# Kernel optimization log

Hardware: AMD Instinct MI355X
Metric: run time of the kernel (lower is better)

The kernel has to match this reference:

```python
import jax, jax.numpy as jnp
import numpy as np

EPS = 1e-5
NEG_SLOPE = 0.2

def _linear(x, w, b):
    return x @ w.T + b

def _seg_softmax(a, dst, n):
    # numerically stable softmax over edges grouped by destination node
    m = jax.ops.segment_max(a, dst, num_segments=n)
    e = jnp.exp(a - m[dst])
    s = jax.ops.segment_sum(e, dst, num_segments=n)
    return e / (s[dst] + 1e-16)

def _gat(x, src, dst, n, w, a_src, a_dst, b):
    # PyG GATConv, heads=1: h = xW^T; alpha = LeakyReLU(a_s.h_src + a_d.h_dst)
    h = x @ w.T                                   # [N,H]
    al_s = (h * a_src).sum(-1)                    # [N]
    al_d = (h * a_dst).sum(-1)                    # [N]
    alpha = jax.nn.leaky_relu(al_s[src] + al_d[dst], NEG_SLOPE)  # [E]
    attn = _seg_softmax(alpha, dst, n)
    out = jax.ops.segment_sum(attn[:, None] * h[src], dst, num_segments=n)
    return out + b

def _bn(x, g, b):
    # BatchNorm over the node dimension (training-style batch stats, eval dropout)
    mu = x.mean(0)
    var = x.var(0)
    return (x - mu) * jax.lax.rsqrt(var + EPS) * g + b

def setup_inputs() -> dict:
    key = jax.random.key(0)
    N, E, SAT, NEI, H, OUT = 50000, 1600000, 32, 32, 128, 16
    ks = jax.random.split(key, 26)
    p = lambda k, shape, s=0.05: jax.random.normal(k, shape, jnp.float32) * s
    return {
        "x": jax.random.normal(ks[0], (N, SAT + NEI), jnp.float32),
        "edge_index": jax.random.randint(ks[1], (2, E), 0, N, jnp.int32),
        "sat_w": p(ks[2], (H, SAT)), "sat_b": jnp.zeros((H,), jnp.float32),
        "neigh_w": p(ks[3], (H, NEI)), "neigh_b": jnp.zeros((H,), jnp.float32),
        "fus_w": p(ks[4], (1, 2 * H)), "fus_b": jnp.zeros((1,), jnp.float32),
        "w1": p(ks[5], (H, H)), "as1": p(ks[6], (H,)), "ad1": p(ks[7], (H,)), "b1": jnp.zeros((H,), jnp.float32),
        "g1": jnp.ones((H,), jnp.float32), "be1": jnp.zeros((H,), jnp.float32),
        "w2": p(ks[8], (H, H)), "as2": p(ks[9], (H,)), "ad2": p(ks[10], (H,)), "b2": jnp.zeros((H,), jnp.float32),
        "g2": jnp.ones((H,), jnp.float32), "be2": jnp.zeros((H,), jnp.float32),
        "fc1_w": p(ks[11], (H, H)), "fc1_b": jnp.zeros((H,), jnp.float32),
        "fc2_w": p(ks[12], (OUT, H)), "fc2_b": jnp.zeros((OUT,), jnp.float32),
    }

def reference(x, edge_index, sat_w, sat_b, neigh_w, neigh_b, fus_w, fus_b,
              w1, as1, ad1, b1, g1, be1, w2, as2, ad2, b2, g2, be2,
              fc1_w, fc1_b, fc2_w, fc2_b):
    n = x.shape[0]
    sat_dim = sat_w.shape[1]
    sat = jax.nn.relu(_linear(x[:, :sat_dim], sat_w, sat_b))
    nei = jax.nn.relu(_linear(x[:, sat_dim:], neigh_w, neigh_b))
    gate = jax.nn.sigmoid(_linear(jnp.concatenate([sat, nei], axis=1), fus_w, fus_b))
    h = gate * sat + (1.0 - gate) * nei
    # GATConv adds self-loops by default
    loops = jnp.arange(n, dtype=edge_index.dtype)
    src = jnp.concatenate([edge_index[0], loops])
    dst = jnp.concatenate([edge_index[1], loops])
    res = h
    h = jax.nn.relu(_bn(_gat(h, src, dst, n, w1, as1, ad1, b1), g1, be1)) + res
    res = h
    h = jax.nn.relu(_bn(_gat(h, src, dst, n, w2, as2, ad2, b2), g2, be2)) + res
    h = jax.nn.relu(_linear(h, fc1_w, fc1_b))
    return _linear(h, fc2_w, fc2_b)
```

## Files before the change

kernel.cpp:

```cpp
#include <hip/hip_runtime.h>

#define H 128

typedef __attribute__((ext_vector_type(8))) short bf16x8;
typedef __attribute__((ext_vector_type(4))) float f32x4;

__device__ __forceinline__ float bf2f(unsigned short u) {
    return __uint_as_float(((unsigned)u) << 16);
}
__device__ __forceinline__ unsigned short f2bf(float f) {
    unsigned u = __float_as_uint(f);
    unsigned r = (u + 0x7fffu + ((u >> 16) & 1u)) >> 16;
    return (unsigned short)r;
}
__device__ __forceinline__ unsigned pack2bf(float a, float b) {
    return (unsigned)f2bf(a) | ((unsigned)f2bf(b) << 16);
}

__global__ void fuse_kernel(const float* __restrict__ x,
                            const float* __restrict__ sat_w, const float* __restrict__ sat_b,
                            const float* __restrict__ neigh_w, const float* __restrict__ neigh_b,
                            const float* __restrict__ fus_w, const float* __restrict__ fus_b,
                            unsigned short* __restrict__ h0b, int N) {
    __shared__ unsigned smem[8512];
    __shared__ float reds[4][64];
    unsigned* a_lds = smem;
    unsigned* w_lds = smem + 2304;
    int tid = threadIdx.x;
    int base = blockIdx.x * 64;
    for (int i = tid; i < 64 * 32; i += 256) {
        int n = i >> 5, kp = i & 31;
        int gn = base + n;
        float2 v = (gn < N) ? *(const float2*)(x + (size_t)gn * 64 + kp * 2) : make_float2(0.f, 0.f);
        a_lds[n * 36 + kp] = pack2bf(v.x, v.y);
    }
    for (int i = tid; i < 256 * 16; i += 256) {
        int r = i >> 4, kp = i & 15;
        const float* wsrc = (r < 128) ? (sat_w + (size_t)r * 32) : (neigh_w + (size_t)(r - 128) * 32);
        float2 v = *(const float2*)(wsrc + kp * 2);
        w_lds[r * 20 + kp] = pack2bf(v.x, v.y);
    }
    __syncthreads();
    int lane = tid & 63;
    int wv = tid >> 6;
    int lr = lane & 15, lk = lane >> 4;
    f32x4 accS[4][2], accN[4][2];
#pragma unroll
    for (int r = 0; r < 4; ++r)
#pragma unroll
        for (int t = 0; t < 2; ++t) {
            accS[r][t] = (f32x4){0.f, 0.f, 0.f, 0.f};
            accN[r][t] = (f32x4){0.f, 0.f, 0.f, 0.f};
        }
    bf16x8 afS[4], afN[4];
#pragma unroll
    for (int r = 0; r < 4; ++r) {
        afS[r] = *(const bf16x8*)&a_lds[(r * 16 + lr) * 36 + lk * 4];
        afN[r] = *(const bf16x8*)&a_lds[(r * 16 + lr) * 36 + 16 + lk * 4];
    }
#pragma unroll
    for (int t = 0; t < 2; ++t) {
        bf16x8 bS = *(const bf16x8*)&w_lds[(wv * 32 + t * 16 + lr) * 20 + lk * 4];
        bf16x8 bN = *(const bf16x8*)&w_lds[(128 + wv * 32 + t * 16 + lr) * 20 + lk * 4];
#pragma unroll
        for (int r = 0; r < 4; ++r) {
            accS[r][t] = __builtin_amdgcn_mfma_f32_16x16x32_bf16(afS[r], bS, accS[r][t], 0, 0, 0);
            accN[r][t] = __builtin_amdgcn_mfma_f32_16x16x32_bf16(afN[r], bN, accN[r][t], 0, 0, 0);
        }
    }
    __syncthreads();
    unsigned short* cst = (unsigned short*)smem;
#pragma unroll
    for (int t = 0; t < 2; ++t) {
        int col = wv * 32 + t * 16 + lr;
        float sb = sat_b[col], nb = neigh_b[col];
#pragma unroll
        for (int r = 0; r < 4; ++r) {
#pragma unroll
            for (int j = 0; j < 4; ++j) {
                int srow = r * 16 + lk * 4 + j;
                cst[srow * 266 + col] = f2bf(fmaxf(accS[r][t][j] + sb, 0.f));
                cst[srow * 266 + 133 + col] = f2bf(fmaxf(accN[r][t][j] + nb, 0.f));
            }
        }
    }
    __syncthreads();
    int node = tid & 63;
    int part = tid >> 6;
    float ps = 0.f;
#pragma unroll
    for (int k = 0; k < 32; ++k) {
        int col = part * 32 + k;
        ps += bf2f(cst[node * 266 + col]) * fus_w[col]
            + bf2f(cst[node * 266 + 133 + col]) * fus_w[128 + col];
    }
    reds[part][node] = ps;
    __syncthreads();
    float tot = reds[0][node] + reds[1][node] + reds[2][node] + reds[3][node];
    float g = 1.f / (1.f + __expf(-(tot + fus_b[0])));
    if (base + node < N) {
        unsigned* op = (unsigned*)h0b + (size_t)(base + node) * 64 + part * 16;
#pragma unroll
        for (int kp = 0; kp < 16; ++kp) {
            int col = part * 32 + kp * 2;
            float o0 = g * bf2f(cst[node * 266 + col]) + (1.f - g) * bf2f(cst[node * 266 + 133 + col]);
            float o1 = g * bf2f(cst[node * 266 + col + 1]) + (1.f - g) * bf2f(cst[node * 266 + 134 + col]);
            op[kp] = pack2bf(o0, o1);
        }
    }
}

template <int TAG, int MODE>
__global__ void gemm128m(const void* __restrict__ inv, const float* __restrict__ w,
                         const float* __restrict__ bias, int do_relu,
                         unsigned short* __restrict__ outb, int N,
                         const float* __restrict__ a_sp, const float* __restrict__ a_dp,
                         float* __restrict__ al_s, float* __restrict__ al_d,
                         const float* __restrict__ bns, const unsigned short* __restrict__ resb,
                         unsigned* __restrict__ yout) {
    __shared__ unsigned a_lds[64 * 68];
    __shared__ unsigned w_lds[128 * 68];
    __shared__ float reds[4][64];
    __shared__ float redd[4][64];
    int tid = threadIdx.x;
    int base = blockIdx.x * 64;
    for (int i = tid; i < 64 * 64; i += 256) {
        int n = i >> 6, kp = i & 63;
        int gn = base + n;
        unsigned p = 0u;
        if (gn < N) {
            if (MODE == 1) {
                p = ((const unsigned*)inv)[(size_t)gn * 64 + kp];
            } else {
                float2 v = *(const float2*)((const float*)inv + (size_t)gn * 128 + kp * 2);
                float2 sc = ((const float2*)bns)[kp];
                float2 sh = ((const float2*)(bns + 128))[kp];
                ushort2 rr = ((const ushort2*)(resb + (size_t)gn * 128))[kp];
                float y0 = fmaxf(v.x * sc.x + sh.x, 0.f) + bf2f(rr.x);
                float y1 = fmaxf(v.y * sc.y + sh.y, 0.f) + bf2f(rr.y);
                p = pack2bf(y0, y1);
                if (yout) yout[(size_t)gn * 64 + kp] = p;
            }
        }
        a_lds[n * 68 + kp] = p;
    }
    for (int i = tid; i < 128 * 64; i += 256) {
        int c = i >> 6, kp = i & 63;
        float2 v = *(const float2*)(w + (size_t)c * 128 + kp * 2);
        w_lds[c * 68 + kp] = pack2bf(v.x, v.y);
    }
    __syncthreads();
    int lane = tid & 63;
    int wv = tid >> 6;
    int lr = lane & 15;
    int lk = lane >> 4;
    f32x4 acc[4][2];
#pragma unroll
    for (int r = 0; r < 4; ++r)
#pragma unroll
        for (int t = 0; t < 2; ++t) acc[r][t] = (f32x4){0.f, 0.f, 0.f, 0.f};
    for (int c = 0; c < 4; ++c) {
        bf16x8 af[4], bfr[2];
#pragma unroll
        for (int r = 0; r < 4; ++r)
            af[r] = *(const bf16x8*)&a_lds[(r * 16 + lr) * 68 + c * 16 + lk * 4];
#pragma unroll
        for (int t = 0; t < 2; ++t)
            bfr[t] = *(const bf16x8*)&w_lds[(wv * 32 + t * 16 + lr) * 68 + c * 16 + lk * 4];
#pragma unroll
        for (int r = 0; r < 4; ++r)
#pragma unroll
            for (int t = 0; t < 2; ++t)
                acc[r][t] = __builtin_amdgcn_mfma_f32_16x16x32_bf16(af[r], bfr[t], acc[r][t], 0, 0, 0);
    }
    __syncthreads();
    unsigned short* cst = (unsigned short*)a_lds;
#pragma unroll
    for (int t = 0; t < 2; ++t) {
        int col = wv * 32 + t * 16 + lr;
        float bv = bias ? bias[col] : 0.f;
#pragma unroll
        for (int r = 0; r < 4; ++r) {
#pragma unroll
            for (int j = 0; j < 4; ++j) {
                float v = acc[r][t][j] + bv;
                if (do_relu) v = fmaxf(v, 0.f);
                cst[(r * 16 + lk * 4 + j) * 136 + col] = f2bf(v);
            }
        }
    }
    __syncthreads();
    for (int i = tid; i < 64 * 64; i += 256) {
        int n = i >> 6, kp = i & 63;
        int gn = base + n;
        if (gn < N) ((unsigned*)outb)[(size_t)gn * 64 + kp] = a_lds[n * 68 + kp];
    }
    if (a_sp) {
        int node = tid & 63;
        int part = tid >> 6;
        float ps = 0.f, pd = 0.f;
        int kb = part * 32;
        const unsigned short* xr = cst + node * 136 + kb;
#pragma unroll
        for (int k = 0; k < 32; ++k) {
            float v = bf2f(xr[k]);
            ps += v * a_sp[kb + k];
            pd += v * a_dp[kb + k];
        }
        reds[part][node] = ps;
        redd[part][node] = pd;
        __syncthreads();
        if (tid < 64) {
            int gn = base + tid;
            if (gn < N) {
                al_s[gn] = reds[0][tid] + reds[1][tid] + reds[2][tid] + reds[3][tid];
                al_d[gn] = redd[0][tid] + redd[1][tid] + redd[2][tid] + redd[3][tid];
            }
        }
    }
}

#define PBMAX 6400
#define NBSTR 256
__global__ void pack_bucket(const int* __restrict__ src, const int* __restrict__ dst,
                            unsigned* __restrict__ pk2, int* __restrict__ cntBB,
                            int* __restrict__ offBB, int E, int PB) {
    __shared__ unsigned opk[PBMAX];
    __shared__ unsigned opk2[PBMAX];
    __shared__ int lcnt[256];
    __shared__ int tmp[256];
    int tid = threadIdx.x;
    int blk = blockIdx.x;
    int e0 = blk * PB;
    int n = min(PB, E - e0);
    if (n < 0) n = 0;
    lcnt[tid] = 0;
    __syncthreads();
    for (int i = tid; i < n; i += 256) {
        int s = src[e0 + i];
        int d = dst[e0 + i];
        unsigned p = ((unsigned)d << 16) | (unsigned)s;
        opk[i] = p;
        atomicAdd(&lcnt[d >> 8], 1);
    }
    __syncthreads();
    int v = lcnt[tid];
    tmp[tid] = v;
    __syncthreads();
    for (int off = 1; off < 256; off <<= 1) {
        int u = (tid >= off) ? tmp[tid - off] : 0;
        __syncthreads();
        tmp[tid] += u;
        __syncthreads();
    }
    int excl = tmp[tid] - v;
    cntBB[(size_t)blk * NBSTR + tid] = v;
    offBB[(size_t)blk * NBSTR + tid] = excl;
    lcnt[tid] = excl;
    __syncthreads();
    for (int i = tid; i < n; i += 256) {
        unsigned p = opk[i];
        int pos = atomicAdd(&lcnt[(p >> 16) >> 8], 1);
        opk2[pos] = p;
    }
    __syncthreads();
    for (int i = tid; i < n; i += 256) pk2[e0 + i] = opk2[i];
}

__global__ void bucket_base(const int* __restrict__ cntBB, int* __restrict__ bbase,
                            int* __restrict__ rowptr, float* __restrict__ accum,
                            int E, int N, int NBLK) {
    __shared__ int tmp[256];
    int tid = threadIdx.x;
    for (int i = tid; i < 4096; i += 256) accum[i] = 0.f;
    int tot = 0;
    for (int blk = 0; blk < NBLK; ++blk) tot += cntBB[(size_t)blk * NBSTR + tid];
    tmp[tid] = tot;
    __syncthreads();
    for (int off = 1; off < 256; off <<= 1) {
        int u = (tid >= off) ? tmp[tid - off] : 0;
        __syncthreads();
        tmp[tid] += u;
        __syncthreads();
    }
    bbase[tid] = tmp[tid] - tot;
    if (tid == 0) rowptr[N] = E;
}

#define BCAP 10240
__global__ void scatter_sort2(const unsigned* __restrict__ pk2, const int* __restrict__ cntBB,
                              const int* __restrict__ offBB, const int* __restrict__ bbase,
                              int* __restrict__ ssrc, int* __restrict__ rowptr,
                              int N, int PB) {
    __shared__ int segoff[257];
    __shared__ int segsrc[256];
    __shared__ int lcur[256];
    __shared__ int tmp[256];
    __shared__ int osrc[BCAP];
    int b = blockIdx.x;
    int d0 = b << 8;
    int tid = threadIdx.x;
    int c = cntBB[(size_t)tid * NBSTR + b];
    segsrc[tid] = tid * PB + offBB[(size_t)tid * NBSTR + b];
    tmp[tid] = c;
    lcur[tid] = 0;
    __syncthreads();
    for (int off = 1; off < 256; off <<= 1) {
        int u = (tid >= off) ? tmp[tid - off] : 0;
        __syncthreads();
        tmp[tid] += u;
        __syncthreads();
    }
    segoff[tid] = tmp[tid] - c;
    if (tid == 255) segoff[256] = tmp[255];
    __syncthreads();
    int cntb = segoff[256];
    for (int i = tid; i < cntb; i += 256) {
        int lo = 0, hi = 255;
        while (lo < hi) { int mid = (lo + hi + 1) >> 1; if (segoff[mid] <= i) lo = mid; else hi = mid - 1; }
        unsigned p = pk2[segsrc[lo] + (i - segoff[lo])];
        atomicAdd(&lcur[(int)(p >> 16) - d0], 1);
    }
    __syncthreads();
    int v = lcur[tid];
    tmp[tid] = v;
    __syncthreads();
    for (int off = 1; off < 256; off <<= 1) {
        int u = (tid >= off) ? tmp[tid - off] : 0;
        __syncthreads();
        tmp[tid] += u;
        __syncthreads();
    }
    int excl = tmp[tid] - v;
    int gbase = bbase[b];
    if (d0 + tid < N) rowptr[d0 + tid] = gbase + excl;
    lcur[tid] = excl;
    __syncthreads();
    for (int i = tid; i < cntb; i += 256) {
        int lo = 0, hi = 255;
        while (lo < hi) { int mid = (lo + hi + 1) >> 1; if (segoff[mid] <= i) lo = mid; else hi = mid - 1; }
        unsigned p = pk2[segsrc[lo] + (i - segoff[lo])];
        int pos = atomicAdd(&lcur[(int)(p >> 16) - d0], 1);
        osrc[pos] = (int)(p & 0xFFFFu);
    }
    __syncthreads();
    for (int i = tid; i < cntb; i += 256) ssrc[gbase + i] = osrc[i];
}

template <int TAG>
__global__ void gat_agg(const int* __restrict__ rowptr, const int* __restrict__ ssrc,
                        const float* __restrict__ al_s, const float* __restrict__ al_d,
                        const unsigned short* __restrict__ hb, float* __restrict__ out,
                        float* __restrict__ accum8, int N) {
    __shared__ int s_sv[4][64];
    __shared__ float s_ev[4][64];
    __shared__ float ys[4][128];
    __shared__ float yq[4][128];
    int tid = threadIdx.x;
    int wiw = tid >> 6;
    int w = (blockIdx.x * blockDim.x + tid) >> 6;
    int lane = tid & 63;
    int sub = lane >> 5;
    int fl = lane & 31;
    float a0 = 0.f, a1 = 0.f, a2 = 0.f, a3 = 0.f;
    float ss = 0.f;
    if (w < N) {
        int beg = rowptr[w], end = rowptr[w + 1];
        float ald = al_d[w];
        float a_self = al_s[w] + ald;
        a_self = (a_self > 0.f) ? a_self : 0.2f * a_self;
        float m = a_self;
        for (int e = beg + lane; e < end; e += 64) {
            float a = al_s[ssrc[e]] + ald;
            a = (a > 0.f) ? a : 0.2f * a;
            m = fmaxf(m, a);
        }
        for (int off = 32; off; off >>= 1) m = fmaxf(m, __shfl_xor(m, off));
        for (int base = beg; base < end; base += 64) {
            int nch = min(64, end - base);
            int sv = 0;
            float ev = 0.f;
            if (lane < nch) {
                sv = ssrc[base + lane];
                float a = al_s[sv] + ald;
                a = (a > 0.f) ? a : 0.2f * a;
                ev = __expf(a - m);
            }
            ss += ev;
            s_sv[wiw][lane] = sv;
            s_ev[wiw][lane] = ev;
            for (int j0 = 0; j0 < nch; j0 += 8) {
                ushort4 hv[4];
                float evv[4];
#pragma unroll
                for (int jj = 0; jj < 4; ++jj) {
                    int j = j0 + 2 * jj + sub;
                    bool ok = j < nch;
                    int svj = ok ? s_sv[wiw][j] : 0;
                    evv[jj] = ok ? s_ev[wiw][j] : 0.f;
                    hv[jj] = ((const ushort4*)(hb + (size_t)svj * H))[fl];
                }
#pragma unroll
                for (int jj = 0; jj < 4; ++jj) {
                    a0 += evv[jj] * bf2f(hv[jj].x);
                    a1 += evv[jj] * bf2f(hv[jj].y);
                    a2 += evv[jj] * bf2f(hv[jj].z);
                    a3 += evv[jj] * bf2f(hv[jj].w);
                }
            }
        }
        for (int off = 32; off; off >>= 1) ss += __shfl_xor(ss, off);
        a0 += __shfl_xor(a0, 32);
        a1 += __shfl_xor(a1, 32);
        a2 += __shfl_xor(a2, 32);
        a3 += __shfl_xor(a3, 32);
        float ev_self = __expf(a_self - m);
        ss += ev_self;
        ushort4 hs = ((const ushort4*)(hb + (size_t)w * H))[fl];
        a0 += ev_self * bf2f(hs.x);
        a1 += ev_self * bf2f(hs.y);
        a2 += ev_self * bf2f(hs.z);
        a3 += ev_self * bf2f(hs.w);
        float inv = 1.f / (ss + 1e-16f);
        a0 *= inv; a1 *= inv; a2 *= inv; a3 *= inv;
        if (sub == 0) {
            ((float4*)(out + (size_t)w * H))[fl] = make_float4(a0, a1, a2, a3);
        }
    }
    if (sub == 0) {
        float4 yy = (w < N) ? make_float4(a0, a1, a2, a3) : make_float4(0.f, 0.f, 0.f, 0.f);
        ((float4*)&ys[wiw][0])[fl] = yy;
        ((float4*)&yq[wiw][0])[fl] = make_float4(yy.x * yy.x, yy.y * yy.y, yy.z * yy.z, yy.w * yy.w);
    }
    __syncthreads();
    if (tid < 128) {
        float s = ys[0][tid] + ys[1][tid] + ys[2][tid] + ys[3][tid];
        float q = yq[0][tid] + yq[1][tid] + yq[2][tid] + yq[3][tid];
        float* ac = accum8 + (size_t)(blockIdx.x & 7) * 256;
        atomicAdd(ac + tid, s);
        atomicAdd(ac + 128 + tid, q);
    }
}

__global__ void bn_finalize(const float* __restrict__ accum8, const float* __restrict__ g,
                            const float* __restrict__ be, float* __restrict__ bns, int N) {
    int tid = threadIdx.x;
    if (tid >= 128) return;
    float s = 0.f, q = 0.f;
#pragma unroll
    for (int c = 0; c < 8; ++c) {
        s += accum8[c * 256 + tid];
        q += accum8[c * 256 + 128 + tid];
    }
    float Ninv = 1.f / (float)N;
    float mu = s * Ninv;
    float var = q * Ninv - mu * mu;
    float rsig = rsqrtf(var + 1e-5f);
    float sc = rsig * g[tid];
    bns[tid] = sc;
    bns[128 + tid] = be[tid] - mu * sc;
}

__global__ void fc2_kernel(const unsigned short* __restrict__ in, const float* __restrict__ w,
                           const float* __restrict__ b, float* __restrict__ out,
                           int N, int OUT) {
    __shared__ float wsm[16 * 132];
    __shared__ float xs[16][129];
    int tid = threadIdx.x;
    for (int i = tid; i < OUT * H; i += 256) {
        int o = i >> 7, k = i & 127;
        wsm[o * 132 + k] = w[i];
    }
    int nb = blockIdx.x * 16;
    for (int i = tid; i < 16 * 128; i += 256) {
        int n = i >> 7, k = i & 127;
        int gn = nb + n;
        xs[n][k] = (gn < N) ? bf2f(in[(size_t)gn * H + k]) : 0.f;
    }
    __syncthreads();
    int o = tid & 15;
    int nn = tid >> 4;
    int n = nb + nn;
    if (n >= N || o >= OUT) return;
    const float* xr = xs[nn];
    const float* wr = wsm + o * 132;
    float acc = b[o];
#pragma unroll 8
    for (int k = 0; k < H; k += 4) {
        acc += xr[k] * wr[k] + xr[k + 1] * wr[k + 1] + xr[k + 2] * wr[k + 2] + xr[k + 3] * wr[k + 3];
    }
    out[(size_t)n * OUT + o] = acc;
}


extern "C" void kernel_launch(void* const* d_in, const int* in_sizes, int n_in,
                              void* d_out, int out_size, void* d_ws, size_t ws_size,
                              hipStream_t stream) {
    const float* x       = (const float*)d_in[0];
    const int*   ei      = (const int*)d_in[1];
    const float* sat_w   = (const float*)d_in[2];
    const float* sat_b   = (const float*)d_in[3];
    const float* neigh_w = (const float*)d_in[4];
    const float* neigh_b = (const float*)d_in[5];
    const float* fus_w   = (const float*)d_in[6];
    const float* fus_b   = (const float*)d_in[7];
    const float* w1      = (const float*)d_in[8];
    const float* as1     = (const float*)d_in[9];
    const float* ad1     = (const float*)d_in[10];
    const float* g1      = (const float*)d_in[12];
    const float* be1     = (const float*)d_in[13];
    const float* w2      = (const float*)d_in[14];
    const float* as2     = (const float*)d_in[15];
    const float* ad2     = (const float*)d_in[16];
    const float* g2      = (const float*)d_in[18];
    const float* be2     = (const float*)d_in[19];
    const float* fc1_w   = (const float*)d_in[20];
    const float* fc1_b   = (const float*)d_in[21];
    const float* fc2_w   = (const float*)d_in[22];
    const float* fc2_b   = (const float*)d_in[23];

    int N = in_sizes[0] / 64;
    int E = in_sizes[1] / 2;
    int OUT = in_sizes[23];
    int PB = (E + 255) / 256;
    int NBUKET = (N + 255) >> 8;

    float* ws    = (float*)d_ws;
    float* h0    = ws;
    float* hA    = h0 + (size_t)N * H;
    float* agg   = hA + (size_t)N * H;
    float* al_s  = agg + (size_t)N * H;
    float* al_d  = al_s + N;
    float* accum = al_d + N;
    float* bns1  = accum + 4096;
    float* bns2  = bns1 + 256;
    int* rowptr  = (int*)(bns2 + 256);
    int* cntBB   = rowptr + (N + 1);
    int* offBB   = cntBB + 256 * NBSTR;
    int* bbase   = offBB + 256 * NBSTR;
    int* ssrc    = bbase + 256;
    unsigned* pk2= (unsigned*)(ssrc + E);
    unsigned* y1b= pk2 + E;
    unsigned short* hAb = (unsigned short*)hA;
    unsigned short* h0b = (unsigned short*)(hA + (size_t)N * 64);

    const int* srcp = ei;
    const int* dstp = ei + E;

    dim3 b256(256);
    int gGemm = (N + 63) / 64;
    int gWaveN = (N + 3) / 4;

    fuse_kernel<<<gGemm, b256, 0, stream>>>(x, sat_w, sat_b, neigh_w, neigh_b, fus_w, fus_b, h0b, N);

    pack_bucket<<<256, b256, 0, stream>>>(srcp, dstp, pk2, cntBB, offBB, E, PB);
    bucket_base<<<1, b256, 0, stream>>>(cntBB, bbase, rowptr, accum, E, N, 256);
    scatter_sort2<<<NBUKET, b256, 0, stream>>>(pk2, cntBB, offBB, bbase, ssrc, rowptr, N, PB);

    gemm128m<1, 1><<<gGemm, b256, 0, stream>>>(h0b, w1, nullptr, 0, hAb, N, as1, ad1, al_s, al_d,
                                               nullptr, nullptr, nullptr);
    gat_agg<1><<<gWaveN, b256, 0, stream>>>(rowptr, ssrc, al_s, al_d, hAb, agg, accum, N);
    bn_finalize<<<1, 128, 0, stream>>>(accum, g1, be1, bns1, N);

    gemm128m<2, 2><<<gGemm, b256, 0, stream>>>(agg, w2, nullptr, 0, hAb, N, as2, ad2, al_s, al_d,
                                               bns1, h0b, y1b);
    gat_agg<2><<<gWaveN, b256, 0, stream>>>(rowptr, ssrc, al_s, al_d, hAb, h0, accum + 2048, N);
    bn_finalize<<<1, 128, 0, stream>>>(accum + 2048, g2, be2, bns2, N);

    gemm128m<3, 2><<<gGemm, b256, 0, stream>>>(h0, fc1_w, fc1_b, 1, hAb, N, nullptr, nullptr,
                                               nullptr, nullptr, bns2, (const unsigned short*)y1b,
                                               nullptr);
    fc2_kernel<<<(N + 15) / 16, b256, 0, stream>>>(hAb, fc2_w, fc2_b, (float*)d_out, N, OUT);
}
```

Baseline: 352.7 us.

## Fuse BN finalize into GEMM, transpose bucket counts, stage bucket edges in LDS

Removes the two single-block bn_finalize launches by having each MODE-2 GEMM block recompute the BatchNorm scale and shift from the accumulated sums into shared memory. Transposes the cntBB/offBB layout so bucket_base can do a wave-parallel coalesced reduction and scatter_sort2 reads contiguous rows. scatter_sort2 now copies each bucket's edge segments into LDS once instead of running a binary search and a global reload in both passes. This adds another 40KB of LDS per scatter block, which may lower occupancy, and every GEMM block redundantly repeats the small BN computation.

Result: slower. 374.7 us (+6.2%).

```diff
diff --git a/kernel.cpp b/kernel.cpp
--- a/kernel.cpp
+++ b/kernel.cpp
@@ -116,14 +116,33 @@
                          unsigned short* __restrict__ outb, int N,
                          const float* __restrict__ a_sp, const float* __restrict__ a_dp,
                          float* __restrict__ al_s, float* __restrict__ al_d,
-                         const float* __restrict__ bns, const unsigned short* __restrict__ resb,
-                         unsigned* __restrict__ yout) {
+                         const float* __restrict__ accum8, const float* __restrict__ gvec,
+                         const float* __restrict__ bevec,
+                         const unsigned short* __restrict__ resb, unsigned* __restrict__ yout) {
     __shared__ unsigned a_lds[64 * 68];
     __shared__ unsigned w_lds[128 * 68];
     __shared__ float reds[4][64];
     __shared__ float redd[4][64];
+    __shared__ float sc_l[128], sh_l[128];
     int tid = threadIdx.x;
     int base = blockIdx.x * 64;
+    if (MODE == 2) {
+        if (tid < 128) {
+            float s = 0.f, q = 0.f;
+#pragma unroll
+            for (int c = 0; c < 8; ++c) {
+                s += accum8[c * 256 + tid];
+                q += accum8[c * 256 + 128 + tid];
+            }
+            float Ninv = 1.f / (float)N;
+            float mu = s * Ninv;
+            float var = q * Ninv - mu * mu;
+            float sc = rsqrtf(var + 1e-5f) * gvec[tid];
+            sc_l[tid] = sc;
+            sh_l[tid] = bevec[tid] - mu * sc;
+        }
+        __syncthreads();
+    }
     for (int i = tid; i < 64 * 64; i += 256) {
         int n = i >> 6, kp = i & 63;
         int gn = base + n;
@@ -133,8 +152,8 @@
                 p = ((const unsigned*)inv)[(size_t)gn * 64 + kp];
             } else {
                 float2 v = *(const float2*)((const float*)inv + (size_t)gn * 128 + kp * 2);
-                float2 sc = ((const float2*)bns)[kp];
-                float2 sh = ((const float2*)(bns + 128))[kp];
+                float2 sc = ((const float2*)sc_l)[kp];
+                float2 sh = ((const float2*)sh_l)[kp];
                 ushort2 rr = ((const ushort2*)(resb + (size_t)gn * 128))[kp];
                 float y0 = fmaxf(v.x * sc.x + sh.x, 0.f) + bf2f(rr.x);
                 float y1 = fmaxf(v.y * sc.y + sh.y, 0.f) + bf2f(rr.y);
@@ -254,8 +273,8 @@
         __syncthreads();
     }
     int excl = tmp[tid] - v;
-    cntBB[(size_t)blk * NBSTR + tid] = v;
-    offBB[(size_t)blk * NBSTR + tid] = excl;
+    cntBB[(size_t)tid * NBSTR + blk] = v;
+    offBB[(size_t)tid * NBSTR + blk] = excl;
     lcnt[tid] = excl;
     __syncthreads();
     for (int i = tid; i < n; i += 256) {
@@ -269,13 +288,20 @@
 
 __global__ void bucket_base(const int* __restrict__ cntBB, int* __restrict__ bbase,
                             int* __restrict__ rowptr, float* __restrict__ accum,
-                            int E, int N, int NBLK) {
+                            int E, int N) {
+    __shared__ int tot[256];
     __shared__ int tmp[256];
-    int tid = threadIdx.x;
+    int tid = threadIdx.x, wv = tid >> 6, lane = tid & 63;
     for (int i = tid; i < 4096; i += 256) accum[i] = 0.f;
-    int tot = 0;
-    for (int blk = 0; blk < NBLK; ++blk) tot += cntBB[(size_t)blk * NBSTR + tid];
-    tmp[tid] = tot;
+    for (int r = wv; r < 256; r += 4) {
+        int s = 0;
+        for (int i = lane; i < 256; i += 64) s += cntBB[(size_t)r * NBSTR + i];
+        for (int off = 32; off; off >>= 1) s += __shfl_xor(s, off);
+        if (lane == 0) tot[r] = s;
+    }
+    __syncthreads();
+    int v = tot[tid];
+    tmp[tid] = v;
     __syncthreads();
     for (int off = 1; off < 256; off <<= 1) {
         int u = (tid >= off) ? tmp[tid - off] : 0;
@@ -283,7 +309,7 @@
         tmp[tid] += u;
         __syncthreads();
     }
-    bbase[tid] = tmp[tid] - tot;
+    bbase[tid] = tmp[tid] - v;
     if (tid == 0) rowptr[N] = E;
 }
 
@@ -294,14 +320,17 @@
                               int N, int PB) {
     __shared__ int segoff[257];
     __shared__ int segsrc[256];
+    __shared__ int segcnt[256];
     __shared__ int lcur[256];
     __shared__ int tmp[256];
+    __shared__ unsigned opk[BCAP];
     __shared__ int osrc[BCAP];
     int b = blockIdx.x;
     int d0 = b << 8;
     int tid = threadIdx.x;
-    int c = cntBB[(size_t)tid * NBSTR + b];
-    segsrc[tid] = tid * PB + offBB[(size_t)tid * NBSTR + b];
+    int c = cntBB[(size_t)b * NBSTR + tid];
+    segcnt[tid] = c;
+    segsrc[tid] = tid * PB + offBB[(size_t)b * NBSTR + tid];
     tmp[tid] = c;
     lcur[tid] = 0;
     __syncthreads();
@@ -311,16 +340,18 @@
         tmp[tid] += u;
         __syncthreads();
     }
-    segoff[tid] = tmp[tid] - c;
+    segoff[tid] = tmp[tid] - segcnt[tid];
     if (tid == 255) segoff[256] = tmp[255];
     __syncthreads();
     int cntb = segoff[256];
-    for (int i = tid; i < cntb; i += 256) {
-        int lo = 0, hi = 255;
-        while (lo < hi) { int mid = (lo + hi + 1) >> 1; if (segoff[mid] <= i) lo = mid; else hi = mid - 1; }
-        unsigned p = pk2[segsrc[lo] + (i - segoff[lo])];
-        atomicAdd(&lcur[(int)(p >> 16) - d0], 1);
-    }
+    int wv = tid >> 6, lane = tid & 63;
+    for (int s = wv; s < 256; s += 4) {
+        int sc = segcnt[s], so = segoff[s], gs = segsrc[s];
+        for (int i = lane; i < sc; i += 64) opk[so + i] = pk2[gs + i];
+    }
+    __syncthreads();
+    for (int i = tid; i < cntb; i += 256)
+        atomicAdd(&lcur[(opk[i] >> 16) & 255], 1);
     __syncthreads();
     int v = lcur[tid];
     tmp[tid] = v;
@@ -337,10 +368,8 @@
     lcur[tid] = excl;
     __syncthreads();
     for (int i = tid; i < cntb; i += 256) {
-        int lo = 0, hi = 255;
-        while (lo < hi) { int mid = (lo + hi + 1) >> 1; if (segoff[mid] <= i) lo = mid; else hi = mid - 1; }
-        unsigned p = pk2[segsrc[lo] + (i - segoff[lo])];
-        int pos = atomicAdd(&lcur[(int)(p >> 16) - d0], 1);
+        unsigned p = opk[i];
+        int pos = atomicAdd(&lcur[(p >> 16) & 255], 1);
         osrc[pos] = (int)(p & 0xFFFFu);
     }
     __syncthreads();
@@ -442,25 +471,6 @@
     }
 }
 
-__global__ void bn_finalize(const float* __restrict__ accum8, const float* __restrict__ g,
-                            const float* __restrict__ be, float* __restrict__ bns, int N) {
-    int tid = threadIdx.x;
-    if (tid >= 128) return;
-    float s = 0.f, q = 0.f;
-#pragma unroll
-    for (int c = 0; c < 8; ++c) {
-        s += accum8[c * 256 + tid];
-        q += accum8[c * 256 + 128 + tid];
-    }
-    float Ninv = 1.f / (float)N;
-    float mu = s * Ninv;
-    float var = q * Ninv - mu * mu;
-    float rsig = rsqrtf(var + 1e-5f);
-    float sc = rsig * g[tid];
-    bns[tid] = sc;
-    bns[128 + tid] = be[tid] - mu * sc;
-}
-
 __global__ void fc2_kernel(const unsigned short* __restrict__ in, const float* __restrict__ w,
                            const float* __restrict__ b, float* __restrict__ out,
                            int N, int OUT) {
@@ -532,9 +542,7 @@
     float* al_s  = agg + (size_t)N * H;
     float* al_d  = al_s + N;
     float* accum = al_d + N;
-    float* bns1  = accum + 4096;
-    float* bns2  = bns1 + 256;
-    int* rowptr  = (int*)(bns2 + 256);
+    int* rowptr  = (int*)(accum + 4096);
     int* cntBB   = rowptr + (N + 1);
     int* offBB   = cntBB + 256 * NBSTR;
     int* bbase   = offBB + 256 * NBSTR;
@@ -554,21 +562,19 @@
     fuse_kernel<<<gGemm, b256, 0, stream>>>(x, sat_w, sat_b, neigh_w, neigh_b, fus_w, fus_b, h0b, N);
 
     pack_bucket<<<256, b256, 0, stream>>>(srcp, dstp, pk2, cntBB, offBB, E, PB);
-    bucket_base<<<1, b256, 0, stream>>>(cntBB, bbase, rowptr, accum, E, N, 256);
+    bucket_base<<<1, b256, 0, stream>>>(cntBB, bbase, rowptr, accum, E, N);
     scatter_sort2<<<NBUKET, b256, 0, stream>>>(pk2, cntBB, offBB, bbase, ssrc, rowptr, N, PB);
 
     gemm128m<1, 1><<<gGemm, b256, 0, stream>>>(h0b, w1, nullptr, 0, hAb, N, as1, ad1, al_s, al_d,
-                                               nullptr, nullptr, nullptr);
+                                               nullptr, nullptr, nullptr, nullptr, nullptr);
     gat_agg<1><<<gWaveN, b256, 0, stream>>>(rowptr, ssrc, al_s, al_d, hAb, agg, accum, N);
-    bn_finalize<<<1, 128, 0, stream>>>(accum, g1, be1, bns1, N);
 
     gemm128m<2, 2><<<gGemm, b256, 0, stream>>>(agg, w2, nullptr, 0, hAb, N, as2, ad2, al_s, al_d,
-                                               bns1, h0b, y1b);
+                                               accum, g1, be1, h0b, y1b);
     gat_agg<2><<<gWaveN, b256, 0, stream>>>(rowptr, ssrc, al_s, al_d, hAb, h0, accum + 2048, N);
-    bn_finalize<<<1, 128, 0, stream>>>(accum + 2048, g2, be2, bns2, N);
 
     gemm128m<3, 2><<<gGemm, b256, 0, stream>>>(h0, fc1_w, fc1_b, 1, hAb, N, nullptr, nullptr,
-                                               nullptr, nullptr, bns2, (const unsigned short*)y1b,
-                                               nullptr);
+                                               nullptr, nullptr, accum + 2048, g2, be2,
+                                               (const unsigned short*)y1b, nullptr);
     fc2_kernel<<<(N + 15) / 16, b256, 0, stream>>>(hAb, fc2_w, fc2_b, (float*)d_out, N, OUT);
 }
```
